# Performance work log

Measured on AMD Instinct MI355X. Metric: run time of the kernel, lower is better.

The kernel has to match this reference:

```python
import jax, jax.numpy as jnp
import numpy as np

B, L, H, ED, NCONV = 64, 2048, 128, 4, 3
N = B * L


def gat(x, src, dst, edge_attr, W, a_s, a_d, We, a_e, b, self_loops):
    """PyG GATConv, heads=1, concat=True, negative_slope=0.2, fill_value='mean'."""
    n = x.shape[0]
    h = x @ W                              # [N,H]
    a_src = h @ a_s                        # [N]
    a_dst = h @ a_d                        # [N]
    alpha = a_src[src] + a_dst[dst] + (edge_attr @ We) @ a_e  # [E]
    if self_loops:
        ones = jnp.ones(src.shape[0], x.dtype)
        deg = jax.ops.segment_sum(ones, dst, num_segments=n)
        mean_attr = jax.ops.segment_sum(edge_attr, dst, num_segments=n) / jnp.maximum(deg, 1.0)[:, None]
        loop_alpha = a_src + a_dst + (mean_attr @ We) @ a_e
        idx = jnp.arange(n, dtype=src.dtype)
        src = jnp.concatenate([src, idx])
        dst = jnp.concatenate([dst, idx])
        alpha = jnp.concatenate([alpha, loop_alpha])
    alpha = jax.nn.leaky_relu(alpha, 0.2)
    m = jax.ops.segment_max(alpha, dst, num_segments=n)
    ex = jnp.exp(alpha - m[dst])
    den = jax.ops.segment_sum(ex, dst, num_segments=n)
    coef = ex / jnp.maximum(den, 1e-16)[dst]
    return jax.ops.segment_sum(coef[:, None] * h[src], dst, num_segments=n) + b


def setup_inputs() -> dict:
    key = jax.random.key(0)
    ks = iter(jax.random.split(key, 32))
    # binary trees: per graph, node k>0 has parent (k-1)//2; edge child->parent (to_up)
    local = np.arange(1, L)
    parent = (local - 1) // 2
    offs = (np.arange(B) * L)[:, None]
    src = jnp.asarray((local[None, :] + offs).ravel(), dtype=jnp.int32)
    dst = jnp.asarray((parent[None, :] + offs).ravel(), dtype=jnp.int32)
    E = src.shape[0]
    s = 0.1
    inp = {
        "x": jax.random.normal(next(ks), (N,), jnp.float32),
        "src": src,
        "dst": dst,
        "edge_attr": jax.random.normal(next(ks), (E, ED), jnp.float32),
        "up_W0": jax.random.normal(next(ks), (1, H)) * s,
        "up_W": jax.random.normal(next(ks), (NCONV - 1, H, H)) * s,
        "up_att_src": jax.random.normal(next(ks), (NCONV, H)) * s,
        "up_att_dst": jax.random.normal(next(ks), (NCONV, H)) * s,
        "up_We": jax.random.normal(next(ks), (NCONV, ED, H)) * s,
        "up_att_edge": jax.random.normal(next(ks), (NCONV, H)) * s,
        "up_b": jax.random.normal(next(ks), (NCONV, H)) * s,
        "down_W": jax.random.normal(next(ks), (NCONV - 1, H, H)) * s,
        "down_att_src": jax.random.normal(next(ks), (NCONV - 1, H)) * s,
        "down_att_dst": jax.random.normal(next(ks), (NCONV - 1, H)) * s,
        "down_We": jax.random.normal(next(ks), (NCONV - 1, ED, H)) * s,
        "down_att_edge": jax.random.normal(next(ks), (NCONV - 1, H)) * s,
        "down_b": jax.random.normal(next(ks), (NCONV - 1, H)) * s,
        "lin_W": jax.random.normal(next(ks), (NCONV - 1, H, H)) * s,
        "lin_b": jax.random.normal(next(ks), (NCONV - 1, H)) * s,
        "lin_last_W": jax.random.normal(next(ks), (H, 1)) * s,
        "lin_last_b": jax.random.normal(next(ks), (1,)) * s,
    }
    return inp


def reference(x, src, dst, edge_attr, up_W0, up_W, up_att_src, up_att_dst, up_We,
              up_att_edge, up_b, down_W, down_att_src, down_att_dst, down_We,
              down_att_edge, down_b, lin_W, lin_b, lin_last_W, lin_last_b):
    h = x[:, None]                                            # flat_c.view(-1,1)
    # upward pass: toup GATConvs (with self loops) + relu
    for i in range(NCONV):
        W = up_W0 if i == 0 else up_W[i - 1]
        h = jax.nn.relu(gat(h, src, dst, edge_attr, W, up_att_src[i], up_att_dst[i],
                            up_We[i], up_att_edge[i], up_b[i], True))
    x_up = h
    # downward pass uses reversed edges, no self loops; replicates original's
    # indexing bug (todown[0] used twice, todown[-1] never used)
    src_d, dst_d = dst, src
    x_down = jax.nn.relu(gat(x_up, src_d, dst_d, edge_attr, down_W[0], down_att_src[0],
                             down_att_dst[0], down_We[0], down_att_edge[0], down_b[0], False))
    xx = x_down + x_up
    for i in range(NCONV - 1):
        xx = jax.nn.relu(xx @ lin_W[i] + lin_b[i])
        x_down = jax.nn.relu(gat(xx, src_d, dst_d, edge_attr, down_W[i], down_att_src[i],
                                 down_att_dst[i], down_We[i], down_att_edge[i], down_b[i], False))
        xx = x_down + x_up
    final_emb = xx
    out_nodes = xx @ lin_last_W + lin_last_b                  # [N,1]
    batch_out = out_nodes.reshape(B, L)                       # all graphs are max_len
    batch_emb = final_emb.reshape(B, L, H)
    out = batch_out - batch_out[:, :1]                        # subtract root node
    return out, batch_emb
```

## Files before the change

kernel.cpp:

```cpp
#include <hip/hip_runtime.h>
#include <hip/hip_bf16.h>
#include <cstdint>
#include <cstddef>

typedef unsigned short u16;
typedef short bf16x8 __attribute__((ext_vector_type(8)));
typedef float f32x4 __attribute__((ext_vector_type(4)));

#define Bn 64
#define Ln 2048
#define Hn 128
#define EDn 4
#define Nn (Bn*Ln)

#define CV_W0    0
#define CV_WUP   128
#define CV_AS    32896
#define CV_AD    33280
#define CV_WE    33664
#define CV_AE    35200
#define CV_BUP   35584
#define CV_WD    35968
#define CV_BD    68736
#define CV_WL    68992
#define CV_BL    101760
#define CV_WLAST 102016
#define CV_TOTAL 102144

__device__ __forceinline__ float b2f(u16 u) {
  union { float f; unsigned int i; } v; v.i = ((unsigned int)u) << 16; return v.f;
}
__device__ __forceinline__ u16 f2b(float f) {
  __hip_bfloat16 h = __float2bfloat16(f);
  union { __hip_bfloat16 h; u16 u; } v; v.h = h; return v.u;
}
__device__ __forceinline__ float lrelu(float v) { return v >= 0.f ? v : 0.2f * v; }
__device__ __forceinline__ float wave_sum(float r) {
  #pragma unroll
  for (int off = 32; off > 0; off >>= 1) r += __shfl_xor(r, off, 64);
  return r;
}
__device__ __forceinline__ float ld_in(const void* p, size_t i, int f) {
  return f ? b2f(((const u16*)p)[i]) : ((const float*)p)[i];
}
__device__ __forceinline__ u16* Cbase(void* dout, int f) {
  return f ? ((u16*)dout + Nn) : (u16*)((float*)dout + Nn);
}
__device__ __forceinline__ float lo16(unsigned v) { return b2f((u16)(v & 0xFFFF)); }
__device__ __forceinline__ float hi16(unsigned v) { return b2f((u16)(v >> 16)); }

__device__ __forceinline__ void gload_lds16(const void* g, void* l) {
  __builtin_amdgcn_global_load_lds(
      (const __attribute__((address_space(1))) void*)g,
      (__attribute__((address_space(3))) void*)l, 16, 0, 0);
}

__device__ __forceinline__ int xcd_remap(int bid, int nwg) {
  return (bid & 7) * (nwg >> 3) + (bid >> 3);
}

__device__ __forceinline__ float2 coef_row(int p, const float2* __restrict__ asr,
                                           const void* __restrict__ edge_attr, int f,
                                           float w0, float w1, float w2, float w3) {
  int local = p & (Ln - 1);
  int root = p - local;
  int nb = p >> 11;
  int c1l = 2*local + 1, c2l = 2*local + 2;
  int deg = (c1l < Ln ? 1 : 0) + (c2l < Ln ? 1 : 0);
  float2 aa = asr[p];
  float e1 = 0.f, e2 = 0.f, sc1 = 0.f, sc2 = 0.f;
  if (deg >= 1) {
    size_t ei = ((size_t)nb*(Ln-1) + (c1l-1))*EDn;
    if (f) {
      ushort4 v = *(const ushort4*)((const u16*)edge_attr + ei);
      e1 = b2f(v.x)*w0 + b2f(v.y)*w1 + b2f(v.z)*w2 + b2f(v.w)*w3;
      if (deg == 2) {
        ushort4 v2 = *(const ushort4*)((const u16*)edge_attr + ei + EDn);
        e2 = b2f(v2.x)*w0 + b2f(v2.y)*w1 + b2f(v2.z)*w2 + b2f(v2.w)*w3;
      }
    } else {
      float4 v = *(const float4*)((const float*)edge_attr + ei);
      e1 = v.x*w0 + v.y*w1 + v.z*w2 + v.w*w3;
      if (deg == 2) {
        float4 v2 = *(const float4*)((const float*)edge_attr + ei + EDn);
        e2 = v2.x*w0 + v2.y*w1 + v2.z*w2 + v2.w*w3;
      }
    }
    sc1 = lrelu(asr[root + c1l].x + aa.y + e1);
    if (deg == 2) sc2 = lrelu(asr[root + c2l].x + aa.y + e2);
  }
  float mean_e = deg ? (e1 + e2) / (float)deg : 0.f;
  float ss = lrelu(aa.x + aa.y + mean_e);
  float m = ss;
  if (deg >= 1) m = fmaxf(m, sc1);
  if (deg == 2) m = fmaxf(m, sc2);
  float es  = __expf(ss - m);
  float ec1 = (deg >= 1) ? __expf(sc1 - m) : 0.f;
  float ec2 = (deg == 2) ? __expf(sc2 - m) : 0.f;
  float inv = 1.f / (es + ec1 + ec2);
  float2 cf; cf.x = ec1 * inv; cf.y = ec2 * inv;
  return cf;
}

__global__ void detect_kernel(const u16* __restrict__ x, int* __restrict__ flag) {
  int lane = threadIdx.x;
  u16 u = x[lane];
  int e = (u >> 7) & 0xFF;
  bool good = (e >= 100 && e <= 140) || ((u & 0x7FFF) == 0);
  unsigned long long m = __ballot(good);
  if (lane == 0) *flag = (__popcll(m) >= 56) ? 1 : 0;
}

struct CvtArgs { const void* src[12]; int off[12]; int tr[12]; };
__global__ void cvt_kernel(CvtArgs a, const int* __restrict__ flagp, u16* __restrict__ dst) {
  int f = *flagp;
  int i = blockIdx.x * 256 + threadIdx.x;
  if (i >= CV_TOTAL) return;
  int s = 0;
  #pragma unroll
  for (int k = 1; k < 12; ++k) s = (i >= a.off[k]) ? k : s;
  int j = i - a.off[s];
  int sj = j;
  if (a.tr[s]) {
    int mat = j >> 14, jm = j & 16383;
    int r = jm >> 7, c = jm & 127;
    int us = c >> 3, sub = c & 7;
    int u = us ^ (r & 15);
    int k = u * 8 + sub;
    sj = (mat << 14) + k * 128 + r;
  }
  dst[i] = f ? ((const u16*)a.src[s])[sj] : f2b(((const float*)a.src[s])[sj]);
}

__global__ void prep_kernel(const u16* __restrict__ cvt, float* __restrict__ P) {
  int lane = threadIdx.x & 63;
  #pragma unroll
  for (int d = 0; d < 14; ++d) {
    int ao, bo;
    if (d == 0)      { ao = CV_W0; bo = CV_AS; }
    else if (d == 1) { ao = CV_W0; bo = CV_AD; }
    else { int i = (d-2) >> 2, e = (d-2) & 3; ao = CV_WE + i*EDn*Hn + e*Hn; bo = CV_AE + i*Hn; }
    float r = b2f(cvt[ao+lane])*b2f(cvt[bo+lane])
            + b2f(cvt[ao+lane+64])*b2f(cvt[bo+lane+64]);
    r = wave_sum(r);
    if (lane == 0) P[d] = r;
  }
}

__global__ void up0_kernel(const void* __restrict__ x, const void* __restrict__ edge_attr,
                           const u16* __restrict__ W0, const u16* __restrict__ b0,
                           const float* __restrict__ Pd,
                           u16* __restrict__ y, const int* __restrict__ flagp) {
  __shared__ float comb[64];
  __shared__ float W0s[Hn];
  __shared__ float b0s[Hn];
  int f = *flagp;
  int t = threadIdx.x;
  if (t < Hn) { W0s[t] = b2f(W0[t]); b0s[t] = b2f(b0[t]); }
  int base = xcd_remap(blockIdx.x, gridDim.x) * 64;
  if (t < 64) {
    int n = base + t;
    int local = n & (Ln - 1);
    int nb = n >> 11;
    int root = n - local;
    float S0 = Pd[0], D0 = Pd[1];
    float w0 = Pd[2], w1 = Pd[3], w2 = Pd[4], w3 = Pd[5];
    float xp = ld_in(x, n, f);
    float ad_p = D0 * xp;
    int c1l = 2*local + 1, c2l = 2*local + 2;
    int deg = (c1l < Ln ? 1 : 0) + (c2l < Ln ? 1 : 0);
    float e1 = 0.f, e2 = 0.f, xc1 = 0.f, xc2 = 0.f, sc1 = 0.f, sc2 = 0.f;
    if (deg >= 1) {
      xc1 = ld_in(x, root + c1l, f);
      size_t ei = ((size_t)nb*(Ln-1) + (c1l-1))*EDn;
      e1 = ld_in(edge_attr, ei+0, f)*w0 + ld_in(edge_attr, ei+1, f)*w1
         + ld_in(edge_attr, ei+2, f)*w2 + ld_in(edge_attr, ei+3, f)*w3;
      sc1 = lrelu(S0*xc1 + ad_p + e1);
    }
    if (deg == 2) {
      xc2 = ld_in(x, root + c2l, f);
      size_t ei = ((size_t)nb*(Ln-1) + (c2l-1))*EDn;
      e2 = ld_in(edge_attr, ei+0, f)*w0 + ld_in(edge_attr, ei+1, f)*w1
         + ld_in(edge_attr, ei+2, f)*w2 + ld_in(edge_attr, ei+3, f)*w3;
      sc2 = lrelu(S0*xc2 + ad_p + e2);
    }
    float mean_e = deg ? (e1 + e2) / (float)deg : 0.f;
    float ss = lrelu(S0*xp + ad_p + mean_e);
    float m = ss;
    if (deg >= 1) m = fmaxf(m, sc1);
    if (deg == 2) m = fmaxf(m, sc2);
    float es  = __expf(ss - m);
    float ec1 = (deg >= 1) ? __expf(sc1 - m) : 0.f;
    float ec2 = (deg == 2) ? __expf(sc2 - m) : 0.f;
    float den = es + ec1 + ec2;
    comb[t] = (es*xp + ec1*xc1 + ec2*xc2) / den;
  }
  __syncthreads();
  u16* out = y + (size_t)base * Hn;
  for (int i = t; i < 64*Hn/4; i += 256) {
    int row = i >> 5;
    int col = (i & 31) * 4;
    float c = comb[row];
    ushort4 st;
    st.x = f2b(fmaxf(c*W0s[col+0] + b0s[col+0], 0.f));
    st.y = f2b(fmaxf(c*W0s[col+1] + b0s[col+1], 0.f));
    st.z = f2b(fmaxf(c*W0s[col+2] + b0s[col+2], 0.f));
    st.w = f2b(fmaxf(c*W0s[col+3] + b0s[col+3], 0.f));
    *(ushort4*)&out[(size_t)i*4] = st;
  }
}

template<int GATHER>
__device__ __forceinline__ void load_x(uint4 (&xf)[2][4], const u16* __restrict__ X,
                                       int wbase, int m, int q) {
  #pragma unroll
  for (int rt = 0; rt < 2; ++rt) {
    int R = wbase + rt*16 + m;
    bool zero = false;
    const uint4* src;
    if (GATHER) {
      int local = R & (Ln - 1);
      if (local == 0) { zero = true; src = (const uint4*)X; }
      else src = (const uint4*)(X + (size_t)((R - local) + ((local - 1) >> 1))*Hn);
    } else {
      src = (const uint4*)(X + (size_t)R*Hn);
    }
    #pragma unroll
    for (int ki = 0; ki < 4; ++ki) {
      uint4 v = src[ki*4 + q];
      if (zero) { v.x = 0; v.y = 0; v.z = 0; v.w = 0; }
      xf[rt][ki] = v;
    }
  }
}

template<int EPI, int ASAD>
__device__ __forceinline__ void compute_tile(
    const uint4 (&xf)[2][4], const u16* Ws, int wbase, int m, int q, int f,
    const u16* __restrict__ bias, const u16* __restrict__ Uarr,
    u16* __restrict__ od, float* __restrict__ emf, int out_mode,
    float2* __restrict__ asad, const u16* __restrict__ avs,
    const u16* __restrict__ avd, float* __restrict__ nodesp) {
  float asv[2] = {0.f, 0.f}, adv[2] = {0.f, 0.f};
  #pragma unroll
  for (int cb = 0; cb < 2; ++cb) {
    f32x4 acc[2][4];
    #pragma unroll
    for (int rt = 0; rt < 2; ++rt)
      #pragma unroll
      for (int c4 = 0; c4 < 4; ++c4) acc[rt][c4] = (f32x4){0.f, 0.f, 0.f, 0.f};
    #pragma unroll
    for (int ki = 0; ki < 4; ++ki) {
      #pragma unroll
      for (int c4 = 0; c4 < 4; ++c4) {
        int ct = cb*4 + c4;
        bf16x8 wf = *(bf16x8*)&Ws[((ct*16 + m)*16 + ((ki*4 + q) ^ m))*8];
        #pragma unroll
        for (int rt = 0; rt < 2; ++rt)
          acc[rt][c4] = __builtin_amdgcn_mfma_f32_16x16x32_bf16(
                          wf, *(bf16x8*)&xf[rt][ki], acc[rt][c4], 0, 0, 0);
      }
    }
    #pragma unroll
    for (int rt = 0; rt < 2; ++rt) {
      int R = wbase + rt*16 + m;
      #pragma unroll
      for (int c4 = 0; c4 < 4; ++c4) {
        int ct = cb*4 + c4;
        int c0 = ct*16 + q*4;
        float o[4];
        #pragma unroll
        for (int r = 0; r < 4; ++r) o[r] = acc[rt][c4][r];
        if (ASAD == 1) {
          ushort4 sv = *(const ushort4*)&avs[c0];
          ushort4 dv = *(const ushort4*)&avd[c0];
          asv[rt] += o[0]*b2f(sv.x) + o[1]*b2f(sv.y) + o[2]*b2f(sv.z) + o[3]*b2f(sv.w);
          adv[rt] += o[0]*b2f(dv.x) + o[1]*b2f(dv.y) + o[2]*b2f(dv.z) + o[3]*b2f(dv.w);
        }
        if (EPI >= 1) {
          ushort4 bv = *(const ushort4*)&bias[c0];
          o[0] = fmaxf(o[0] + b2f(bv.x), 0.f); o[1] = fmaxf(o[1] + b2f(bv.y), 0.f);
          o[2] = fmaxf(o[2] + b2f(bv.z), 0.f); o[3] = fmaxf(o[3] + b2f(bv.w), 0.f);
        }
        if (EPI == 2) {
          ushort4 uv = *(const ushort4*)&Uarr[(size_t)R*Hn + c0];
          o[0] += b2f(uv.x); o[1] += b2f(uv.y); o[2] += b2f(uv.z); o[3] += b2f(uv.w);
        }
        if (ASAD == 2) {
          ushort4 sv = *(const ushort4*)&avs[c0];
          asv[rt] += o[0]*b2f(sv.x) + o[1]*b2f(sv.y) + o[2]*b2f(sv.z) + o[3]*b2f(sv.w);
        }
        if (out_mode == 2 && !f) {
          float4 fv; fv.x = o[0]; fv.y = o[1]; fv.z = o[2]; fv.w = o[3];
          *(float4*)&emf[(size_t)R*Hn + c0] = fv;
        } else {
          ushort4 st; st.x = f2b(o[0]); st.y = f2b(o[1]); st.z = f2b(o[2]); st.w = f2b(o[3]);
          *(ushort4*)&od[(size_t)R*Hn + c0] = st;
        }
      }
    }
  }
  #pragma unroll
  for (int rt = 0; rt < 2; ++rt) {
    int R = wbase + rt*16 + m;
    if (ASAD == 1) {
      float as_ = asv[rt], ad_ = adv[rt];
      as_ += __shfl_xor(as_, 16, 64); as_ += __shfl_xor(as_, 32, 64);
      ad_ += __shfl_xor(ad_, 16, 64); ad_ += __shfl_xor(ad_, 32, 64);
      if (q == 0) { float2 v; v.x = as_; v.y = ad_; asad[R] = v; }
    }
    if (ASAD == 2) {
      float as_ = asv[rt];
      as_ += __shfl_xor(as_, 16, 64); as_ += __shfl_xor(as_, 32, 64);
      if (q == 0) nodesp[R] = as_;
    }
  }
}

template<int GATHER, int EPI, int ASAD>
__global__ __launch_bounds__(256, 3) void gemm_k(
                       const u16* __restrict__ Xp, const u16* __restrict__ Wt,
                       const u16* __restrict__ bias, const u16* __restrict__ Uarr,
                       u16* __restrict__ outp, void* __restrict__ dout,
                       const int* __restrict__ flagp, int x_is_C, int out_mode,
                       float2* __restrict__ asad, const u16* __restrict__ avs,
                       const u16* __restrict__ avd, float* __restrict__ nodesp) {
  __shared__ u16 Ws[Hn*Hn];
  int f = *flagp;
  const u16* X = x_is_C ? Cbase(dout, f) : Xp;
  int t = threadIdx.x;
  int lane = t & 63, w = t >> 6;
  int m = lane & 15, q = lane >> 4;
  int row0 = xcd_remap(blockIdx.x, gridDim.x) * 256;
  int wb0 = row0 + w*32;
  int wb1 = row0 + 128 + w*32;
  #pragma unroll
  for (int i = 0; i < 8; ++i)
    gload_lds16(Wt + (size_t)(i*256 + t)*8, &Ws[(size_t)(i*256 + (t & ~63))*8]);
  uint4 xf0[2][4];
  load_x<GATHER>(xf0, X, wb0, m, q);
  __syncthreads();
  uint4 xf1[2][4];
  load_x<GATHER>(xf1, X, wb1, m, q);
  u16* Cb = Cbase(dout, f);
  float* emf = (float*)dout + Nn;
  u16* od = (out_mode == 0) ? outp : (out_mode == 1 ? Cb : (u16*)dout + Nn);
  compute_tile<EPI, ASAD>(xf0, Ws, wb0, m, q, f, bias, Uarr, od, emf, out_mode,
                          asad, avs, avd, nodesp);
  compute_tile<EPI, ASAD>(xf1, Ws, wb1, m, q, f, bias, Uarr, od, emf, out_mode,
                          asad, avs, avd, nodesp);
}

__global__ __launch_bounds__(256, 4) void gemm_blend_k(
                       const u16* __restrict__ Wt, const void* __restrict__ edge_attr,
                       const float2* __restrict__ asad_in, const float* __restrict__ Pd,
                       const u16* __restrict__ bias_up, u16* __restrict__ outp,
                       void* __restrict__ dout, const int* __restrict__ flagp,
                       float2* __restrict__ asad2, const u16* __restrict__ avs,
                       const u16* __restrict__ avd) {
  __shared__ u16 Ws[Hn*Hn];
  int f = *flagp;
  const u16* h = Cbase(dout, f);
  int t = threadIdx.x;
  int lane = t & 63, w = t >> 6;
  int m = lane & 15, q = lane >> 4;
  int row0 = xcd_remap(blockIdx.x, gridDim.x) * 128;
  int wbase = row0 + w*32;
  float we0 = Pd[6], we1 = Pd[7], we2 = Pd[8], we3 = Pd[9];
  #pragma unroll
  for (int i = 0; i < 8; ++i)
    gload_lds16(Wt + (size_t)(i*256 + t)*8, &Ws[(size_t)(i*256 + (t & ~63))*8]);
  uint4 xf[2][4];
  #pragma unroll
  for (int rt = 0; rt < 2; ++rt) {
    int R = wbase + rt*16 + m;
    int local = R & (Ln - 1);
    int root = R - local;
    int c1l = 2*local + 1, c2l = 2*local + 2;
    int r1 = (c1l < Ln) ? root + c1l : R;
    int r2 = (c2l < Ln) ? root + c2l : R;
    float2 cf = coef_row(R, asad_in, edge_attr, f, we0, we1, we2, we3);
    float es = 1.f - cf.x - cf.y;
    const uint4* hp = (const uint4*)(h + (size_t)R*Hn);
    const uint4* h1 = (const uint4*)(h + (size_t)r1*Hn);
    const uint4* h2 = (const uint4*)(h + (size_t)r2*Hn);
    #pragma unroll
    for (int ki = 0; ki < 4; ++ki) {
      int u = ki*4 + q;
      uint4 a = hp[u], b = h1[u], c = h2[u];
      uint4 bv = ((const uint4*)bias_up)[u];
      uint4 st;
      #pragma unroll
      for (int i = 0; i < 4; ++i) {
        unsigned av = ((unsigned*)&a)[i], b1v = ((unsigned*)&b)[i];
        unsigned b2v = ((unsigned*)&c)[i], bbv = ((unsigned*)&bv)[i];
        float o0 = es*lo16(av) + cf.x*lo16(b1v) + cf.y*lo16(b2v) + lo16(bbv);
        float o1 = es*hi16(av) + cf.x*hi16(b1v) + cf.y*hi16(b2v) + hi16(bbv);
        ((unsigned*)&st)[i] = (unsigned)f2b(fmaxf(o0, 0.f))
                            | ((unsigned)f2b(fmaxf(o1, 0.f)) << 16);
      }
      xf[rt][ki] = st;
    }
  }
  __syncthreads();
  float asv[2] = {0.f, 0.f}, adv[2] = {0.f, 0.f};
  #pragma unroll
  for (int cb = 0; cb < 2; ++cb) {
    f32x4 acc[2][4];
    #pragma unroll
    for (int rt = 0; rt < 2; ++rt)
      #pragma unroll
      for (int c4 = 0; c4 < 4; ++c4) acc[rt][c4] = (f32x4){0.f, 0.f, 0.f, 0.f};
    #pragma unroll
    for (int ki = 0; ki < 4; ++ki) {
      #pragma unroll
      for (int c4 = 0; c4 < 4; ++c4) {
        int ct = cb*4 + c4;
        bf16x8 wf = *(bf16x8*)&Ws[((ct*16 + m)*16 + ((ki*4 + q) ^ m))*8];
        #pragma unroll
        for (int rt = 0; rt < 2; ++rt)
          acc[rt][c4] = __builtin_amdgcn_mfma_f32_16x16x32_bf16(
                          wf, *(bf16x8*)&xf[rt][ki], acc[rt][c4], 0, 0, 0);
      }
    }
    #pragma unroll
    for (int rt = 0; rt < 2; ++rt) {
      int R = wbase + rt*16 + m;
      #pragma unroll
      for (int c4 = 0; c4 < 4; ++c4) {
        int ct = cb*4 + c4;
        int c0 = ct*16 + q*4;
        float o0 = acc[rt][c4][0], o1 = acc[rt][c4][1];
        float o2 = acc[rt][c4][2], o3 = acc[rt][c4][3];
        ushort4 sv = *(const ushort4*)&avs[c0];
        ushort4 dv = *(const ushort4*)&avd[c0];
        asv[rt] += o0*b2f(sv.x) + o1*b2f(sv.y) + o2*b2f(sv.z) + o3*b2f(sv.w);
        adv[rt] += o0*b2f(dv.x) + o1*b2f(dv.y) + o2*b2f(dv.z) + o3*b2f(dv.w);
        ushort4 st; st.x = f2b(o0); st.y = f2b(o1); st.z = f2b(o2); st.w = f2b(o3);
        *(ushort4*)&outp[(size_t)R*Hn + c0] = st;
      }
    }
  }
  #pragma unroll
  for (int rt = 0; rt < 2; ++rt) {
    int R = wbase + rt*16 + m;
    float as_ = asv[rt], ad_ = adv[rt];
    as_ += __shfl_xor(as_, 16, 64); as_ += __shfl_xor(as_, 32, 64);
    ad_ += __shfl_xor(ad_, 16, 64); ad_ += __shfl_xor(ad_, 32, 64);
    if (q == 0) { float2 v; v.x = as_; v.y = ad_; asad2[R] = v; }
  }
}

__global__ __launch_bounds__(512, 4) void fused_down_lin_k(
                       const u16* __restrict__ Xp, const u16* __restrict__ Wdt,
                       const u16* __restrict__ bd, const u16* __restrict__ Uarr,
                       const u16* __restrict__ Wlt, const u16* __restrict__ bl,
                       u16* __restrict__ outp) {
  __shared__ u16 Ws[Hn*Hn];
  __shared__ u16 XX[128*Hn];
  int t = threadIdx.x;
  int lane = t & 63, w = t >> 6;
  int m = lane & 15, q = lane >> 4;
  int row0 = xcd_remap(blockIdx.x, gridDim.x) * 128;
  int R = row0 + w*16 + m;
  int rl = w*16 + m;
  #pragma unroll
  for (int i = 0; i < 4; ++i)
    gload_lds16(Wdt + (size_t)(i*512 + t)*8, &Ws[(size_t)(i*512 + (t & ~63))*8]);
  uint4 xf[4];
  {
    int local = R & (Ln - 1);
    bool zero = (local == 0);
    const uint4* src = zero ? (const uint4*)Xp
                     : (const uint4*)(Xp + (size_t)((R - local) + ((local - 1) >> 1))*Hn);
    #pragma unroll
    for (int ki = 0; ki < 4; ++ki) {
      uint4 v = src[ki*4 + q];
      if (zero) { v.x = 0; v.y = 0; v.z = 0; v.w = 0; }
      xf[ki] = v;
    }
  }
  __syncthreads();
  f32x4 acc[8];
  #pragma unroll
  for (int ct = 0; ct < 8; ++ct) acc[ct] = (f32x4){0.f, 0.f, 0.f, 0.f};
  #pragma unroll
  for (int ki = 0; ki < 4; ++ki) {
    #pragma unroll
    for (int ct = 0; ct < 8; ++ct) {
      bf16x8 wf = *(bf16x8*)&Ws[((ct*16 + m)*16 + ((ki*4 + q) ^ m))*8];
      acc[ct] = __builtin_amdgcn_mfma_f32_16x16x32_bf16(
                    wf, *(bf16x8*)&xf[ki], acc[ct], 0, 0, 0);
    }
  }
  __syncthreads();
  #pragma unroll
  for (int i = 0; i < 4; ++i)
    gload_lds16(Wlt + (size_t)(i*512 + t)*8, &Ws[(size_t)(i*512 + (t & ~63))*8]);
  #pragma unroll
  for (int ct = 0; ct < 8; ++ct) {
    int c0 = ct*16 + q*4;
    ushort4 bv = *(const ushort4*)&bd[c0];
    ushort4 uv = *(const ushort4*)&Uarr[(size_t)R*Hn + c0];
    float o0 = fmaxf(acc[ct][0] + b2f(bv.x), 0.f) + b2f(uv.x);
    float o1 = fmaxf(acc[ct][1] + b2f(bv.y), 0.f) + b2f(uv.y);
    float o2 = fmaxf(acc[ct][2] + b2f(bv.z), 0.f) + b2f(uv.z);
    float o3 = fmaxf(acc[ct][3] + b2f(bv.w), 0.f) + b2f(uv.w);
    int uu = (2*ct + (q >> 1)) ^ m;
    uint2 pk;
    pk.x = (unsigned)f2b(o0) | ((unsigned)f2b(o1) << 16);
    pk.y = (unsigned)f2b(o2) | ((unsigned)f2b(o3) << 16);
    *(uint2*)&XX[rl*Hn + uu*8 + (q & 1)*4] = pk;
  }
  __syncthreads();
  f32x4 acc2[8];
  #pragma unroll
  for (int ct = 0; ct < 8; ++ct) acc2[ct] = (f32x4){0.f, 0.f, 0.f, 0.f};
  #pragma unroll
  for (int ki = 0; ki < 4; ++ki) {
    #pragma unroll
    for (int ct = 0; ct < 8; ++ct) {
      bf16x8 wf = *(bf16x8*)&Ws[((ct*16 + m)*16 + ((ki*4 + q) ^ m))*8];
      bf16x8 xb = *(bf16x8*)&XX[rl*Hn + (((ki*4 + q) ^ m))*8];
      acc2[ct] = __builtin_amdgcn_mfma_f32_16x16x32_bf16(wf, xb, acc2[ct], 0, 0, 0);
    }
  }
  #pragma unroll
  for (int ct = 0; ct < 8; ++ct) {
    int c0 = ct*16 + q*4;
    ushort4 bv = *(const ushort4*)&bl[c0];
    ushort4 st;
    st.x = f2b(fmaxf(acc2[ct][0] + b2f(bv.x), 0.f));
    st.y = f2b(fmaxf(acc2[ct][1] + b2f(bv.y), 0.f));
    st.z = f2b(fmaxf(acc2[ct][2] + b2f(bv.z), 0.f));
    st.w = f2b(fmaxf(acc2[ct][3] + b2f(bv.w), 0.f));
    *(ushort4*)&outp[(size_t)R*Hn + c0] = st;
  }
}

__global__ void blend_kernel(const u16* __restrict__ h, const void* __restrict__ edge_attr,
                             const float2* __restrict__ asad2, const float* __restrict__ Pd,
                             const u16* __restrict__ bias, u16* __restrict__ y,
                             const int* __restrict__ flagp) {
  int f = *flagp;
  int t = threadIdx.x;
  int g = t & 15;
  int p = xcd_remap(blockIdx.x, gridDim.x) * 16 + (t >> 4);
  int local = p & (Ln - 1);
  int root = p - local;
  int c1l = 2*local + 1, c2l = 2*local + 2;
  int deg = (c1l < Ln ? 1 : 0) + (c2l < Ln ? 1 : 0);
  float2 cf = coef_row(p, asad2, edge_attr, f, Pd[10], Pd[11], Pd[12], Pd[13]);
  float es = 1.f - cf.x - cf.y;
  int off = g * 8;
  uint4 hp = *(const uint4*)&h[(size_t)p*Hn + off];
  uint4 h1 = {0,0,0,0}, h2 = {0,0,0,0};
  if (deg >= 1) h1 = *(const uint4*)&h[(size_t)(root + c1l)*Hn + off];
  if (deg == 2) h2 = *(const uint4*)&h[(size_t)(root + c2l)*Hn + off];
  uint4 bv = *(const uint4*)&bias[off];
  uint4 st;
  #pragma unroll
  for (int i = 0; i < 4; ++i) {
    unsigned a = ((unsigned*)&hp)[i], b1 = ((unsigned*)&h1)[i];
    unsigned b2 = ((unsigned*)&h2)[i], bb = ((unsigned*)&bv)[i];
    float o0 = es*lo16(a) + cf.x*lo16(b1) + cf.y*lo16(b2) + lo16(bb);
    float o1 = es*hi16(a) + cf.x*hi16(b1) + cf.y*hi16(b2) + hi16(bb);
    ((unsigned*)&st)[i] = (unsigned)f2b(fmaxf(o0, 0.f)) | ((unsigned)f2b(fmaxf(o1, 0.f)) << 16);
  }
  *(uint4*)&y[(size_t)p*Hn + off] = st;
}

__global__ void score_kernel(const float* __restrict__ nodes, void* __restrict__ dout,
                             const int* __restrict__ flagp) {
  int f = *flagp;
  int n = xcd_remap(blockIdx.x, gridDim.x) * 256 + threadIdx.x;
  float v = nodes[n] - nodes[n & ~(Ln - 1)];
  if (f) ((u16*)dout)[n] = f2b(v);
  else   ((float*)dout)[n] = v;
}

extern "C" void kernel_launch(void* const* d_in, const int* in_sizes, int n_in,
                              void* d_out, int out_size, void* d_ws, size_t ws_size,
                              hipStream_t stream) {
  const void* x         = d_in[0];
  const void* edge_attr = d_in[3];

  u16* Ubuf = (u16*)d_ws;
  u16* Abuf = Ubuf + (size_t)Nn*Hn;
  u16* Bbuf = Abuf + (size_t)Nn*Hn;
  u16* cvt  = Bbuf + (size_t)Nn*Hn;
  float2* asad  = (float2*)(cvt + CV_TOTAL);
  float2* asad2 = asad + Nn;
  float* nodes = (float*)(asad2 + Nn);
  int* flag = (int*)(nodes + Nn);
  float* Pdots = (float*)(flag + 4);

  detect_kernel<<<1, 64, 0, stream>>>((const u16*)d_in[0], flag);

  CvtArgs ca;
  ca.src[0]  = d_in[4];  ca.off[0]  = CV_W0;    ca.tr[0]  = 0;
  ca.src[1]  = d_in[5];  ca.off[1]  = CV_WUP;   ca.tr[1]  = 1;
  ca.src[2]  = d_in[6];  ca.off[2]  = CV_AS;    ca.tr[2]  = 0;
  ca.src[3]  = d_in[7];  ca.off[3]  = CV_AD;    ca.tr[3]  = 0;
  ca.src[4]  = d_in[8];  ca.off[4]  = CV_WE;    ca.tr[4]  = 0;
  ca.src[5]  = d_in[9];  ca.off[5]  = CV_AE;    ca.tr[5]  = 0;
  ca.src[6]  = d_in[10]; ca.off[6]  = CV_BUP;   ca.tr[6]  = 0;
  ca.src[7]  = d_in[11]; ca.off[7]  = CV_WD;    ca.tr[7]  = 1;
  ca.src[8]  = d_in[16]; ca.off[8]  = CV_BD;    ca.tr[8]  = 0;
  ca.src[9]  = d_in[17]; ca.off[9]  = CV_WL;    ca.tr[9]  = 1;
  ca.src[10] = d_in[18]; ca.off[10] = CV_BL;    ca.tr[10] = 0;
  ca.src[11] = d_in[19]; ca.off[11] = CV_WLAST; ca.tr[11] = 0;
  cvt_kernel<<<(CV_TOTAL + 255)/256, 256, 0, stream>>>(ca, flag, cvt);
  prep_kernel<<<1, 64, 0, stream>>>(cvt, Pdots);

  up0_kernel<<<Nn/64, 256, 0, stream>>>(x, edge_attr, cvt+CV_W0, cvt+CV_BUP,
                                        Pdots, Abuf, flag);
  gemm_k<0,0,1><<<Nn/256, 256, 0, stream>>>(Abuf, cvt+CV_WUP, nullptr, nullptr,
                                         nullptr, d_out, flag, 0, 1,
                                         asad, cvt+CV_AS+Hn, cvt+CV_AD+Hn, nullptr);
  gemm_blend_k<<<Nn/128, 256, 0, stream>>>(cvt+CV_WUP+Hn*Hn, edge_attr, asad, Pdots,
                                           cvt+CV_BUP+Hn, Bbuf, d_out, flag,
                                           asad2, cvt+CV_AS+2*Hn, cvt+CV_AD+2*Hn);
  blend_kernel<<<Nn/16, 256, 0, stream>>>(Bbuf, edge_attr, asad2, Pdots,
                                          cvt+CV_BUP+2*Hn, Ubuf, flag);

  fused_down_lin_k<<<Nn/128, 512, 0, stream>>>(Ubuf, cvt+CV_WD, cvt+CV_BD, Ubuf,
                                               cvt+CV_WL, cvt+CV_BL, Abuf);
  fused_down_lin_k<<<Nn/128, 512, 0, stream>>>(Abuf, cvt+CV_WD, cvt+CV_BD, Ubuf,
                                               cvt+CV_WL+Hn*Hn, cvt+CV_BL+Hn, Bbuf);
  gemm_k<1,2,2><<<Nn/256, 256, 0, stream>>>(Bbuf, cvt+CV_WD+Hn*Hn, cvt+CV_BD+Hn, Ubuf,
                                         nullptr, d_out, flag, 0, 2,
                                         nullptr, cvt+CV_WLAST, nullptr, nodes);

  score_kernel<<<Nn/256, 256, 0, stream>>>(nodes, d_out, flag);
}
```

Before: 279.5 us.

## Stage tree parent/child rows in LDS for gather GEMMs and blend

```diff
diff --git a/kernel.cpp b/kernel.cpp
--- a/kernel.cpp
+++ b/kernel.cpp
@@ -210,24 +210,29 @@
   }
 }
 
-template<int GATHER>
 __device__ __forceinline__ void load_x(uint4 (&xf)[2][4], const u16* __restrict__ X,
                                        int wbase, int m, int q) {
   #pragma unroll
   for (int rt = 0; rt < 2; ++rt) {
     int R = wbase + rt*16 + m;
-    bool zero = false;
-    const uint4* src;
-    if (GATHER) {
-      int local = R & (Ln - 1);
-      if (local == 0) { zero = true; src = (const uint4*)X; }
-      else src = (const uint4*)(X + (size_t)((R - local) + ((local - 1) >> 1))*Hn);
-    } else {
-      src = (const uint4*)(X + (size_t)R*Hn);
-    }
+    const uint4* src = (const uint4*)(X + (size_t)R*Hn);
+    #pragma unroll
+    for (int ki = 0; ki < 4; ++ki) xf[rt][ki] = src[ki*4 + q];
+  }
+}
+
+__device__ __forceinline__ void read_pw(uint4 (&xf)[2][4], const u16* PW,
+                                        int wbase, int p0l, int m, int q) {
+  #pragma unroll
+  for (int rt = 0; rt < 2; ++rt) {
+    int R = wbase + rt*16 + m;
+    int l = R & (Ln - 1);
+    bool zero = (l == 0);
+    int pr = zero ? 0 : (((l - 1) >> 1) - p0l);
     #pragma unroll
     for (int ki = 0; ki < 4; ++ki) {
-      uint4 v = src[ki*4 + q];
+      int u = ki*4 + q;
+      uint4 v = *(const uint4*)&PW[((size_t)pr*16 + (u ^ (pr & 15)))*8];
       if (zero) { v.x = 0; v.y = 0; v.z = 0; v.w = 0; }
       xf[rt][ki] = v;
     }
@@ -241,6 +246,16 @@
     u16* __restrict__ od, float* __restrict__ emf, int out_mode,
     float2* __restrict__ asad, const u16* __restrict__ avs,
     const u16* __restrict__ avd, float* __restrict__ nodesp) {
+  ushort4 uvr[2][8];
+  if (EPI == 2) {
+    #pragma unroll
+    for (int rt = 0; rt < 2; ++rt) {
+      int R = wbase + rt*16 + m;
+      #pragma unroll
+      for (int ct = 0; ct < 8; ++ct)
+        uvr[rt][ct] = *(const ushort4*)&Uarr[(size_t)R*Hn + ct*16 + q*4];
+    }
+  }
   float asv[2] = {0.f, 0.f}, adv[2] = {0.f, 0.f};
   #pragma unroll
   for (int cb = 0; cb < 2; ++cb) {
@@ -283,7 +298,7 @@
           o[2] = fmaxf(o[2] + b2f(bv.z), 0.f); o[3] = fmaxf(o[3] + b2f(bv.w), 0.f);
         }
         if (EPI == 2) {
-          ushort4 uv = *(const ushort4*)&Uarr[(size_t)R*Hn + c0];
+          ushort4 uv = uvr[rt][ct];
           o[0] += b2f(uv.x); o[1] += b2f(uv.y); o[2] += b2f(uv.z); o[3] += b2f(uv.w);
         }
         if (ASAD == 2) {
@@ -318,14 +333,15 @@
 }
 
 template<int GATHER, int EPI, int ASAD>
-__global__ __launch_bounds__(256, 3) void gemm_k(
+__global__ __launch_bounds__(256, 2) void gemm_k(
                        const u16* __restrict__ Xp, const u16* __restrict__ Wt,
                        const u16* __restrict__ bias, const u16* __restrict__ Uarr,
                        u16* __restrict__ outp, void* __restrict__ dout,
                        const int* __restrict__ flagp, int x_is_C, int out_mode,
                        float2* __restrict__ asad, const u16* __restrict__ avs,
                        const u16* __restrict__ avd, float* __restrict__ nodesp) {
-  __shared__ u16 Ws[Hn*Hn];
+  __shared__ u16 Ws[Hn*Hn + (GATHER ? 130*Hn : 0)];
+  u16* PW = Ws + Hn*Hn;
   int f = *flagp;
   const u16* X = x_is_C ? Cbase(dout, f) : Xp;
   int t = threadIdx.x;
@@ -337,11 +353,30 @@
   #pragma unroll
   for (int i = 0; i < 8; ++i)
     gload_lds16(Wt + (size_t)(i*256 + t)*8, &Ws[(size_t)(i*256 + (t & ~63))*8]);
-  uint4 xf0[2][4];
-  load_x<GATHER>(xf0, X, wb0, m, q);
+  uint4 xf0[2][4], xf1[2][4];
+  int p0l = 0;
+  if (GATHER) {
+    int l0 = row0 & (Ln - 1);
+    p0l = l0 ? ((l0 >> 1) - 1) : 0;
+    size_t pbase = (size_t)((row0 - l0) + p0l) * Hn;
+    for (int i = 0; i < 9; ++i) {
+      int s = i*256 + t;
+      if (s < 129*16) {
+        int r = s >> 4, v = s & 15;
+        gload_lds16(X + pbase + (size_t)r*Hn + (size_t)((v ^ (r & 15))*8),
+                    &PW[(size_t)(i*256 + (t & ~63))*8]);
+      }
+    }
+  } else {
+    load_x(xf0, X, wb0, m, q);
+  }
   __syncthreads();
-  uint4 xf1[2][4];
-  load_x<GATHER>(xf1, X, wb1, m, q);
+  if (GATHER) {
+    read_pw(xf0, PW, wb0, p0l, m, q);
+    read_pw(xf1, PW, wb1, p0l, m, q);
+  } else {
+    load_x(xf1, X, wb1, m, q);
+  }
   u16* Cb = Cbase(dout, f);
   float* emf = (float*)dout + Nn;
   u16* od = (out_mode == 0) ? outp : (out_mode == 1 ? Cb : (u16*)dout + Nn);
@@ -351,7 +386,7 @@
                           asad, avs, avd, nodesp);
 }
 
-__global__ __launch_bounds__(256, 4) void gemm_blend_k(
+__global__ __launch_bounds__(256, 2) void gemm_blend_k(
                        const u16* __restrict__ Wt, const void* __restrict__ edge_attr,
                        const float2* __restrict__ asad_in, const float* __restrict__ Pd,
                        const u16* __restrict__ bias_up, u16* __restrict__ outp,
@@ -359,96 +394,91 @@
                        float2* __restrict__ asad2, const u16* __restrict__ avs,
                        const u16* __restrict__ avd) {
   __shared__ u16 Ws[Hn*Hn];
+  __shared__ u16 CW[Hn*Hn];
   int f = *flagp;
   const u16* h = Cbase(dout, f);
   int t = threadIdx.x;
   int lane = t & 63, w = t >> 6;
   int m = lane & 15, q = lane >> 4;
-  int row0 = xcd_remap(blockIdx.x, gridDim.x) * 128;
-  int wbase = row0 + w*32;
-  float we0 = Pd[6], we1 = Pd[7], we2 = Pd[8], we3 = Pd[9];
+  int row0 = xcd_remap(blockIdx.x, gridDim.x) * 64;
+  int l0 = row0 & (Ln - 1);
+  int root = row0 - l0;
+  int j = w*16 + m;
+  int R = row0 + j;
+  int l = l0 + j;
+  int deg = (2*l+1 < Ln ? 1 : 0) + (2*l+2 < Ln ? 1 : 0);
   #pragma unroll
   for (int i = 0; i < 8; ++i)
     gload_lds16(Wt + (size_t)(i*256 + t)*8, &Ws[(size_t)(i*256 + (t & ~63))*8]);
-  uint4 xf[2][4];
-  #pragma unroll
-  for (int rt = 0; rt < 2; ++rt) {
-    int R = wbase + rt*16 + m;
-    int local = R & (Ln - 1);
-    int root = R - local;
-    int c1l = 2*local + 1, c2l = 2*local + 2;
-    int r1 = (c1l < Ln) ? root + c1l : R;
-    int r2 = (c2l < Ln) ? root + c2l : R;
-    float2 cf = coef_row(R, asad_in, edge_attr, f, we0, we1, we2, we3);
-    float es = 1.f - cf.x - cf.y;
-    const uint4* hp = (const uint4*)(h + (size_t)R*Hn);
-    const uint4* h1 = (const uint4*)(h + (size_t)r1*Hn);
-    const uint4* h2 = (const uint4*)(h + (size_t)r2*Hn);
-    #pragma unroll
-    for (int ki = 0; ki < 4; ++ki) {
-      int u = ki*4 + q;
-      uint4 a = hp[u], b = h1[u], c = h2[u];
-      uint4 bv = ((const uint4*)bias_up)[u];
-      uint4 st;
-      #pragma unroll
-      for (int i = 0; i < 4; ++i) {
-        unsigned av = ((unsigned*)&a)[i], b1v = ((unsigned*)&b)[i];
-        unsigned b2v = ((unsigned*)&c)[i], bbv = ((unsigned*)&bv)[i];
-        float o0 = es*lo16(av) + cf.x*lo16(b1v) + cf.y*lo16(b2v) + lo16(bbv);
-        float o1 = es*hi16(av) + cf.x*hi16(b1v) + cf.y*hi16(b2v) + hi16(bbv);
-        ((unsigned*)&st)[i] = (unsigned)f2b(fmaxf(o0, 0.f))
-                            | ((unsigned)f2b(fmaxf(o1, 0.f)) << 16);
-      }
-      xf[rt][ki] = st;
-    }
-  }
+  if (l0 < Ln/2) {
+    size_t cbase = (size_t)(root + 2*l0 + 1) * Hn;
+    size_t emax = (size_t)Nn*Hn - 8;
+    #pragma unroll
+    for (int i = 0; i < 8; ++i) {
+      int s = i*256 + t;
+      int r = s >> 4, v = s & 15;
+      size_t elem = cbase + (size_t)r*Hn + (size_t)((v ^ (r & 15))*8);
+      if (elem > emax) elem = emax;
+      gload_lds16(h + elem, &CW[(size_t)(i*256 + (t & ~63))*8]);
+    }
+  }
+  uint4 own[4], bv4[4];
+  #pragma unroll
+  for (int ki = 0; ki < 4; ++ki) {
+    own[ki] = *(const uint4*)&h[(size_t)R*Hn + (size_t)((ki*4 + q)*8)];
+    bv4[ki] = ((const uint4*)bias_up)[ki*4 + q];
+  }
+  float2 cf = coef_row(R, asad_in, edge_attr, f, Pd[6], Pd[7], Pd[8], Pd[9]);
+  float es = 1.f - cf.x - cf.y;
   __syncthreads();
-  float asv[2] = {0.f, 0.f}, adv[2] = {0.f, 0.f};
-  #pragma unroll
-  for (int cb = 0; cb < 2; ++cb) {
-    f32x4 acc[2][4];
-    #pragma unroll
-    for (int rt = 0; rt < 2; ++rt)
-      #pragma unroll
-      for (int c4 = 0; c4 < 4; ++c4) acc[rt][c4] = (f32x4){0.f, 0.f, 0.f, 0.f};
-    #pragma unroll
-    for (int ki = 0; ki < 4; ++ki) {
-      #pragma unroll
-      for (int c4 = 0; c4 < 4; ++c4) {
-        int ct = cb*4 + c4;
-        bf16x8 wf = *(bf16x8*)&Ws[((ct*16 + m)*16 + ((ki*4 + q) ^ m))*8];
-        #pragma unroll
-        for (int rt = 0; rt < 2; ++rt)
-          acc[rt][c4] = __builtin_amdgcn_mfma_f32_16x16x32_bf16(
-                          wf, *(bf16x8*)&xf[rt][ki], acc[rt][c4], 0, 0, 0);
-      }
-    }
-    #pragma unroll
-    for (int rt = 0; rt < 2; ++rt) {
-      int R = wbase + rt*16 + m;
-      #pragma unroll
-      for (int c4 = 0; c4 < 4; ++c4) {
-        int ct = cb*4 + c4;
-        int c0 = ct*16 + q*4;
-        float o0 = acc[rt][c4][0], o1 = acc[rt][c4][1];
-        float o2 = acc[rt][c4][2], o3 = acc[rt][c4][3];
-        ushort4 sv = *(const ushort4*)&avs[c0];
-        ushort4 dv = *(const ushort4*)&avd[c0];
-        asv[rt] += o0*b2f(sv.x) + o1*b2f(sv.y) + o2*b2f(sv.z) + o3*b2f(sv.w);
-        adv[rt] += o0*b2f(dv.x) + o1*b2f(dv.y) + o2*b2f(dv.z) + o3*b2f(dv.w);
-        ushort4 st; st.x = f2b(o0); st.y = f2b(o1); st.z = f2b(o2); st.w = f2b(o3);
-        *(ushort4*)&outp[(size_t)R*Hn + c0] = st;
-      }
-    }
-  }
-  #pragma unroll
-  for (int rt = 0; rt < 2; ++rt) {
-    int R = wbase + rt*16 + m;
-    float as_ = asv[rt], ad_ = adv[rt];
-    as_ += __shfl_xor(as_, 16, 64); as_ += __shfl_xor(as_, 32, 64);
-    ad_ += __shfl_xor(ad_, 16, 64); ad_ += __shfl_xor(ad_, 32, 64);
-    if (q == 0) { float2 v; v.x = as_; v.y = ad_; asad2[R] = v; }
-  }
+  int r1 = 2*j, r2 = 2*j + 1;
+  uint4 xf[4];
+  #pragma unroll
+  for (int ki = 0; ki < 4; ++ki) {
+    int u = ki*4 + q;
+    uint4 b = {0,0,0,0}, c = {0,0,0,0};
+    if (deg >= 1) b = *(const uint4*)&CW[((size_t)r1*16 + (u ^ (r1 & 15)))*8];
+    if (deg == 2) c = *(const uint4*)&CW[((size_t)r2*16 + (u ^ (r2 & 15)))*8];
+    uint4 a = own[ki], bb = bv4[ki];
+    uint4 st;
+    #pragma unroll
+    for (int i = 0; i < 4; ++i) {
+      unsigned av = ((unsigned*)&a)[i], b1v = ((unsigned*)&b)[i];
+      unsigned b2v = ((unsigned*)&c)[i], bbv = ((unsigned*)&bb)[i];
+      float o0 = es*lo16(av) + cf.x*lo16(b1v) + cf.y*lo16(b2v) + lo16(bbv);
+      float o1 = es*hi16(av) + cf.x*hi16(b1v) + cf.y*hi16(b2v) + hi16(bbv);
+      ((unsigned*)&st)[i] = (unsigned)f2b(fmaxf(o0, 0.f))
+                          | ((unsigned)f2b(fmaxf(o1, 0.f)) << 16);
+    }
+    xf[ki] = st;
+  }
+  f32x4 acc[8];
+  #pragma unroll
+  for (int ct = 0; ct < 8; ++ct) acc[ct] = (f32x4){0.f, 0.f, 0.f, 0.f};
+  #pragma unroll
+  for (int ki = 0; ki < 4; ++ki) {
+    #pragma unroll
+    for (int ct = 0; ct < 8; ++ct) {
+      bf16x8 wf = *(bf16x8*)&Ws[((ct*16 + m)*16 + ((ki*4 + q) ^ m))*8];
+      acc[ct] = __builtin_amdgcn_mfma_f32_16x16x32_bf16(
+                    wf, *(bf16x8*)&xf[ki], acc[ct], 0, 0, 0);
+    }
+  }
+  float asv = 0.f, adv = 0.f;
+  #pragma unroll
+  for (int ct = 0; ct < 8; ++ct) {
+    int c0 = ct*16 + q*4;
+    float o0 = acc[ct][0], o1 = acc[ct][1], o2 = acc[ct][2], o3 = acc[ct][3];
+    ushort4 sv = *(const ushort4*)&avs[c0];
+    ushort4 dv = *(const ushort4*)&avd[c0];
+    asv += o0*b2f(sv.x) + o1*b2f(sv.y) + o2*b2f(sv.z) + o3*b2f(sv.w);
+    adv += o0*b2f(dv.x) + o1*b2f(dv.y) + o2*b2f(dv.z) + o3*b2f(dv.w);
+    ushort4 st; st.x = f2b(o0); st.y = f2b(o1); st.z = f2b(o2); st.w = f2b(o3);
+    *(ushort4*)&outp[(size_t)R*Hn + c0] = st;
+  }
+  asv += __shfl_xor(asv, 16, 64); asv += __shfl_xor(asv, 32, 64);
+  adv += __shfl_xor(adv, 16, 64); adv += __shfl_xor(adv, 32, 64);
+  if (q == 0) { float2 v; v.x = asv; v.y = adv; asad2[R] = v; }
 }
 
 __global__ __launch_bounds__(512, 4) void fused_down_lin_k(
@@ -457,30 +487,47 @@
                        const u16* __restrict__ Wlt, const u16* __restrict__ bl,
                        u16* __restrict__ outp) {
   __shared__ u16 Ws[Hn*Hn];
-  __shared__ u16 XX[128*Hn];
+  __shared__ u16 XX[Hn*Hn];
+  u16* PW = XX;
   int t = threadIdx.x;
   int lane = t & 63, w = t >> 6;
   int m = lane & 15, q = lane >> 4;
   int row0 = xcd_remap(blockIdx.x, gridDim.x) * 128;
+  int l0 = row0 & (Ln - 1);
+  int root = row0 - l0;
+  int p0l = l0 ? ((l0 >> 1) - 1) : 0;
   int R = row0 + w*16 + m;
   int rl = w*16 + m;
   #pragma unroll
   for (int i = 0; i < 4; ++i)
     gload_lds16(Wdt + (size_t)(i*512 + t)*8, &Ws[(size_t)(i*512 + (t & ~63))*8]);
+  {
+    size_t pbase = (size_t)(root + p0l) * Hn;
+    for (int i = 0; i < 3; ++i) {
+      int s = i*512 + t;
+      if (s < 65*16) {
+        int r = s >> 4, v = s & 15;
+        gload_lds16(Xp + pbase + (size_t)r*Hn + (size_t)((v ^ (r & 15))*8),
+                    &PW[(size_t)(i*512 + (t & ~63))*8]);
+      }
+    }
+  }
+  ushort4 uvr[8];
+  #pragma unroll
+  for (int ct = 0; ct < 8; ++ct)
+    uvr[ct] = *(const ushort4*)&Uarr[(size_t)R*Hn + ct*16 + q*4];
+  __syncthreads();
+  int l = R & (Ln - 1);
+  bool zero = (l == 0);
+  int pr = zero ? 0 : (((l - 1) >> 1) - p0l);
   uint4 xf[4];
-  {
-    int local = R & (Ln - 1);
-    bool zero = (local == 0);
-    const uint4* src = zero ? (const uint4*)Xp
-                     : (const uint4*)(Xp + (size_t)((R - local) + ((local - 1) >> 1))*Hn);
-    #pragma unroll
-    for (int ki = 0; ki < 4; ++ki) {
-      uint4 v = src[ki*4 + q];
-      if (zero) { v.x = 0; v.y = 0; v.z = 0; v.w = 0; }
-      xf[ki] = v;
-    }
-  }
-  __syncthreads();
+  #pragma unroll
+  for (int ki = 0; ki < 4; ++ki) {
+    int u = ki*4 + q;
+    uint4 v = *(const uint4*)&PW[((size_t)pr*16 + (u ^ (pr & 15)))*8];
+    if (zero) { v.x = 0; v.y = 0; v.z = 0; v.w = 0; }
+    xf[ki] = v;
+  }
   f32x4 acc[8];
   #pragma unroll
   for (int ct = 0; ct < 8; ++ct) acc[ct] = (f32x4){0.f, 0.f, 0.f, 0.f};
@@ -501,7 +548,7 @@
   for (int ct = 0; ct < 8; ++ct) {
     int c0 = ct*16 + q*4;
     ushort4 bv = *(const ushort4*)&bd[c0];
-    ushort4 uv = *(const ushort4*)&Uarr[(size_t)R*Hn + c0];
+    ushort4 uv = uvr[ct];
     float o0 = fmaxf(acc[ct][0] + b2f(bv.x), 0.f) + b2f(uv.x);
     float o1 = fmaxf(acc[ct][1] + b2f(bv.y), 0.f) + b2f(uv.y);
     float o2 = fmaxf(acc[ct][2] + b2f(bv.z), 0.f) + b2f(uv.z);
@@ -618,7 +665,7 @@
   gemm_k<0,0,1><<<Nn/256, 256, 0, stream>>>(Abuf, cvt+CV_WUP, nullptr, nullptr,
                                          nullptr, d_out, flag, 0, 1,
                                          asad, cvt+CV_AS+Hn, cvt+CV_AD+Hn, nullptr);
-  gemm_blend_k<<<Nn/128, 256, 0, stream>>>(cvt+CV_WUP+Hn*Hn, edge_attr, asad, Pdots,
+  gemm_blend_k<<<Nn/64, 256, 0, stream>>>(cvt+CV_WUP+Hn*Hn, edge_attr, asad, Pdots,
                                            cvt+CV_BUP+Hn, Bbuf, d_out, flag,
                                            asad2, cvt+CV_AS+2*Hn, cvt+CV_AD+2*Hn);
   blend_kernel<<<Nn/16, 256, 0, stream>>>(Bbuf, edge_attr, asad2, Pdots,
```

Result: no change. 279.5 us (+0.0%).
